# Optimization experiments

Measured on AMD Instinct MI355X. Metric: run time of the kernel, lower is better.

Reference implementation:

```python
import jax, jax.numpy as jnp
import numpy as np

TOP_K = 2


def setup_inputs() -> dict:
    key = jax.random.key(0)
    k1, k2, k3, k4 = jax.random.split(key, 4)
    B, S, H, I, E = 8, 2048, 768, 3072, 8
    x = jax.random.normal(k1, (B, S, H), dtype=jnp.float32)
    # kaiming_uniform-ish scale for weights
    router_w = jax.random.uniform(k2, (E, H), dtype=jnp.float32, minval=-1.0, maxval=1.0) * (1.0 / np.sqrt(H))
    up_w = jax.random.uniform(k3, (E, H, I), dtype=jnp.float32, minval=-1.0, maxval=1.0) * (1.0 / np.sqrt(H))
    down_w = jax.random.uniform(k4, (E, I, H), dtype=jnp.float32, minval=-1.0, maxval=1.0) * (1.0 / np.sqrt(I))
    return {"x": x, "router_w": router_w, "up_w": up_w, "down_w": down_w}


def reference(x, router_w, up_w, down_w):
    B, S, H = x.shape
    E = up_w.shape[0]
    T = B * S
    xf = x.reshape(T, H)
    # router: Linear(H -> E, bias=False) then softmax, top-k, renormalize
    logits = xf @ router_w.T                      # [T, E]
    probs = jax.nn.softmax(logits, axis=-1)
    top_w, top_i = jax.lax.top_k(probs, TOP_K)    # [T, K]
    top_w = top_w / jnp.sum(top_w, axis=-1, keepdims=True)
    # dense per-(token, expert) gate: zero for unselected experts
    gate = jnp.zeros((T, E), dtype=xf.dtype).at[jnp.arange(T)[:, None], top_i].add(top_w)
    # combine: sum_e gate[:, e] * down_e(gelu(up_e(x)))
    out = jnp.zeros_like(xf)
    for e in range(E):  # fixed small expert count; loop is structural, not over data dims
        h = jax.nn.gelu(xf @ up_w[e], approximate=False)   # exact GELU == torch F.gelu
        out = out + gate[:, e:e + 1] * (h @ down_w[e])
    return out.reshape(B, S, H)
```

## Files before the change

### kernel.cpp

```cpp
#include <hip/hip_runtime.h>

typedef short bf16x8 __attribute__((ext_vector_type(8)));
typedef float f32x4  __attribute__((ext_vector_type(4)));

#define T_TOK 16384
#define HD 768
#define ID 3072
#define NE 8
#define NT1MAX 136

__device__ __forceinline__ unsigned short f2bf(float f) {
    unsigned int u = __float_as_uint(f);
    unsigned int r = (u + 0x7FFFu + ((u >> 16) & 1u)) >> 16;
    return (unsigned short)r;
}

__device__ __forceinline__ void gload16(const void* g, void* l) {
    __builtin_amdgcn_global_load_lds(
        (const __attribute__((address_space(1))) void*)g,
        (__attribute__((address_space(3))) void*)l, 16, 0, 0);
}

__device__ __forceinline__ float gelu_f(float x) {
    float z = fabsf(x) * 0.70710678118f;
    float t = 1.0f / fmaf(0.3275911f, z, 1.0f);
    float p = t * fmaf(t, fmaf(t, fmaf(t, fmaf(t, 1.061405429f, -1.453152027f),
                                       1.421413741f), -0.284496736f), 0.254829592f);
    float e = 1.0f - p * __expf(-z * z);
    float erfv = (x >= 0.f) ? e : -e;
    return 0.5f * x * (1.0f + erfv);
}

__device__ __forceinline__ int xcd_swz(int bid, int nwg) {
    int q = nwg >> 3, rr = nwg & 7;
    int xcd = bid & 7, seq = bid >> 3;
    return (xcd < rr ? xcd * (q + 1) : rr * (q + 1) + (xcd - rr) * q) + seq;
}

__global__ __launch_bounds__(256) void k_cvt_x(const float* __restrict__ x,
                                               unsigned short* __restrict__ xb) {
    int i = blockIdx.x * 256 + threadIdx.x;
    float4 v = ((const float4*)x)[i];
    ushort4 o;
    o.x = f2bf(v.x); o.y = f2bf(v.y); o.z = f2bf(v.z); o.w = f2bf(v.w);
    ((ushort4*)xb)[i] = o;
}

__global__ __launch_bounds__(256) void k_tp(const float* __restrict__ in,
                                            unsigned short* __restrict__ out,
                                            int R, int C) {
    __shared__ float t[64][65];
    const float* ine = in + (size_t)blockIdx.z * R * C;
    unsigned short* oute = out + (size_t)blockIdx.z * R * C;
    int c0 = blockIdx.x * 64, r0 = blockIdx.y * 64;
    int lc = threadIdx.x & 63, lr4 = threadIdx.x >> 6;
#pragma unroll
    for (int i = 0; i < 16; i++) {
        int r = i * 4 + lr4;
        t[r][lc] = ine[(size_t)(r0 + r) * C + c0 + lc];
    }
    __syncthreads();
#pragma unroll
    for (int i = 0; i < 16; i++) {
        int r = i * 4 + lr4;
        oute[(size_t)(c0 + r) * R + r0 + lc] = f2bf(t[lc][r]);
    }
}

__global__ __launch_bounds__(256) void k_router(const float* __restrict__ x,
                                                const float* __restrict__ rw,
                                                int* __restrict__ topE,
                                                float* __restrict__ topW) {
    __shared__ float lrw[NE * HD];
    for (int i = threadIdx.x; i < NE * HD; i += 256) lrw[i] = rw[i];
    __syncthreads();
    int lane = threadIdx.x & 63;
    int t = blockIdx.x * 4 + (threadIdx.x >> 6);
    const float* xr = x + (size_t)t * HD;
    float acc[NE] = {0, 0, 0, 0, 0, 0, 0, 0};
    for (int h = lane; h < HD; h += 64) {
        float xv = xr[h];
#pragma unroll
        for (int e = 0; e < NE; e++) acc[e] = fmaf(xv, lrw[e * HD + h], acc[e]);
    }
#pragma unroll
    for (int e = 0; e < NE; e++) {
        float v = acc[e];
#pragma unroll
        for (int o = 32; o > 0; o >>= 1) v += __shfl_xor(v, o, 64);
        acc[e] = v;
    }
    if (lane == 0) {
        int e1 = 0; float l1 = acc[0];
#pragma unroll
        for (int e = 1; e < NE; e++) if (acc[e] > l1) { l1 = acc[e]; e1 = e; }
        int e2 = -1; float l2 = -1e30f;
#pragma unroll
        for (int e = 0; e < NE; e++) if (e != e1 && acc[e] > l2) { l2 = acc[e]; e2 = e; }
        float ex = expf(l2 - l1);
        float w1 = 1.0f / (1.0f + ex);
        topE[2 * t] = e1; topE[2 * t + 1] = e2;
        topW[2 * t] = w1; topW[2 * t + 1] = ex * w1;
    }
}

__global__ __launch_bounds__(256) void k_scatter(const int* __restrict__ topE,
                                                 const float* __restrict__ topW,
                                                 int* __restrict__ counts,
                                                 int* __restrict__ tokL,
                                                 float* __restrict__ gateL) {
    __shared__ int lc[NE], lbase[NE];
    if (threadIdx.x < NE) lc[threadIdx.x] = 0;
    __syncthreads();
    int t = blockIdx.x * 256 + threadIdx.x;
    int e1 = topE[2 * t], e2 = topE[2 * t + 1];
    int p1 = atomicAdd(&lc[e1], 1);
    int p2 = atomicAdd(&lc[e2], 1);
    __syncthreads();
    if (threadIdx.x < NE) lbase[threadIdx.x] = atomicAdd(&counts[threadIdx.x], lc[threadIdx.x]);
    __syncthreads();
    int q1 = lbase[e1] + p1, q2 = lbase[e2] + p2;
    tokL[e1 * T_TOK + q1] = t;  gateL[e1 * T_TOK + q1] = topW[2 * t];
    tokL[e2 * T_TOK + q2] = t;  gateL[e2 * T_TOK + q2] = topW[2 * t + 1];
}

__global__ void k_desc(const int* __restrict__ counts, int* __restrict__ tileE,
                       int* __restrict__ tileM0) {
    if (threadIdx.x == 0 && blockIdx.x == 0) {
        int tl = 0;
        for (int e = 0; e < NE; e++) {
            int c = counts[e];
            int nt = (c + 255) >> 8;
            for (int t = 0; t < nt; t++) { tileE[tl] = e; tileM0[tl] = t << 8; tl++; }
        }
        for (; tl < NT1MAX; tl++) { tileE[tl] = -1; tileM0[tl] = 0; }
    }
}

__global__ __launch_bounds__(512, 2) void k_gemm1(
    const unsigned short* __restrict__ xb,
    const unsigned short* __restrict__ upt,
    const int* __restrict__ tokL,
    const int* __restrict__ counts,
    const int* __restrict__ tileE,
    const int* __restrict__ tileM0,
    unsigned short* __restrict__ h,
    int seg, int ntn, int ldh) {
    __shared__ __align__(16) char lds[4][32768];
    constexpr int NK = HD / 32;
    int L = xcd_swz(blockIdx.x, gridDim.x);
    int mt = L / ntn, ntl = L - mt * ntn;
    int e = tileE[mt];
    if (e < 0) return;
    int m0 = tileM0[mt];
    int nrow = min(256, counts[e] - m0);
    const int* tok = tokL + e * T_TOK + m0;
    int n0 = (seg * ntn + ntl) * 256;

    const int tid = threadIdx.x, lane = tid & 63, wid = tid >> 6;
    const int wm = wid >> 2, wn = wid & 3;
    const int g = lane >> 4, r = lane & 15;

    int ar0 = wid * 16 + r;
    int ar1 = 128 + wid * 16 + r;
    const char* a0 = (const char*)(xb + (size_t)tok[ar0 < nrow ? ar0 : 0] * HD);
    const char* a1 = (const char*)(xb + (size_t)tok[ar1 < nrow ? ar1 : 0] * HD);
    const char* bsl = (const char*)(upt + (size_t)e * ID * HD);
    const char* b0 = bsl + (size_t)(n0 + wid * 16 + r) * (HD * 2);
    const char* b1 = bsl + (size_t)(n0 + 128 + wid * 16 + r) * (HD * 2);
    const int dst = wid * 1024;
    const int koff = g * 16;

    auto issue = [&](int step, int slot) {
        char* base = &lds[slot][0];
        int kb = step * 64 + koff;
        gload16(a0 + kb, base + dst);
        gload16(a1 + kb, base + 8192 + dst);
        gload16(b0 + kb, base + 16384 + dst);
        gload16(b1 + kb, base + 24576 + dst);
    };

    f32x4 acc[8][4];
#pragma unroll
    for (int m = 0; m < 8; m++)
#pragma unroll
        for (int n = 0; n < 4; n++) acc[m][n] = (f32x4){0.f, 0.f, 0.f, 0.f};

    issue(0, 0); issue(1, 1); issue(2, 2);
    asm volatile("s_waitcnt vmcnt(8)" ::: "memory");
    __builtin_amdgcn_s_barrier();
    asm volatile("" ::: "memory");

    const int aoff = wm * 8192 + g * 256 + r * 16;
    const int boff = 16384 + wn * 4096 + g * 256 + r * 16;

    for (int k = 0; k < NK; k++) {
        char* base = &lds[k & 3][0];
        bf16x8 a[4], b[4];
#pragma unroll
        for (int n = 0; n < 4; n++) b[n] = *(const bf16x8*)(base + boff + n * 1024);
#pragma unroll
        for (int m = 0; m < 4; m++) a[m] = *(const bf16x8*)(base + aoff + m * 1024);
        issue(min(k + 3, NK - 1), (k + 3) & 3);
        __builtin_amdgcn_s_setprio(1);
#pragma unroll
        for (int m = 0; m < 4; m++)
#pragma unroll
            for (int n = 0; n < 4; n++)
                acc[m][n] = __builtin_amdgcn_mfma_f32_16x16x32_bf16(a[m], b[n], acc[m][n], 0, 0, 0);
        __builtin_amdgcn_s_setprio(0);
#pragma unroll
        for (int m = 0; m < 4; m++) a[m] = *(const bf16x8*)(base + aoff + (4 + m) * 1024);
        __builtin_amdgcn_s_setprio(1);
#pragma unroll
        for (int m = 0; m < 4; m++)
#pragma unroll
            for (int n = 0; n < 4; n++)
                acc[4 + m][n] = __builtin_amdgcn_mfma_f32_16x16x32_bf16(a[m], b[n], acc[4 + m][n], 0, 0, 0);
        __builtin_amdgcn_s_setprio(0);
        asm volatile("s_waitcnt vmcnt(8)" ::: "memory");
        __builtin_amdgcn_s_barrier();
        asm volatile("" ::: "memory");
    }
    asm volatile("s_waitcnt vmcnt(0)" ::: "memory");

#pragma unroll
    for (int m = 0; m < 8; m++)
#pragma unroll
        for (int j = 0; j < 4; j++) {
            int rl = wm * 128 + m * 16 + g * 4 + j;
            if (rl < nrow) {
                unsigned short* hr = h + (size_t)(mt * 256 + rl) * ldh + ntl * 256 + wn * 64 + r;
#pragma unroll
                for (int n = 0; n < 4; n++) hr[n * 16] = f2bf(gelu_f(acc[m][n][j]));
            }
        }
}

__global__ __launch_bounds__(512, 2) void k_gemm2(
    const unsigned short* __restrict__ h,
    const unsigned short* __restrict__ dnt,
    const int* __restrict__ tokL,
    const float* __restrict__ gateL,
    const int* __restrict__ counts,
    const int* __restrict__ tileE,
    const int* __restrict__ tileM0,
    float* __restrict__ out,
    int seg, int ldh, int nk) {
    __shared__ __align__(16) char lds[4][32768];
    int L = xcd_swz(blockIdx.x, gridDim.x);
    int mt = L / 3, ntl = L - mt * 3;
    int e = tileE[mt];
    if (e < 0) return;
    int m0 = tileM0[mt];
    int nrow = min(256, counts[e] - m0);
    const int* tok = tokL + e * T_TOK + m0;
    const float* gat = gateL + e * T_TOK + m0;
    int n0 = ntl * 256;

    const int tid = threadIdx.x, lane = tid & 63, wid = tid >> 6;
    const int wm = wid >> 2, wn = wid & 3;
    const int g = lane >> 4, r = lane & 15;

    int ar0 = wid * 16 + r;
    int ar1 = 128 + wid * 16 + r;
    const char* a0 = (const char*)h + ((size_t)(mt * 256 + ar0) * ldh) * 2;
    const char* a1 = (const char*)h + ((size_t)(mt * 256 + ar1) * ldh) * 2;
    const char* bsl = (const char*)(dnt + (size_t)e * ID * HD) + (size_t)seg * ldh * 2;
    const char* b0 = bsl + (size_t)(n0 + wid * 16 + r) * (ID * 2);
    const char* b1 = bsl + (size_t)(n0 + 128 + wid * 16 + r) * (ID * 2);
    const int dst = wid * 1024;
    const int koff = g * 16;

    auto issue = [&](int step, int slot) {
        char* base = &lds[slot][0];
        int kb = step * 64 + koff;
        gload16(a0 + kb, base + dst);
        gload16(a1 + kb, base + 8192 + dst);
        gload16(b0 + kb, base + 16384 + dst);
        gload16(b1 + kb, base + 24576 + dst);
    };

    f32x4 acc[8][4];
#pragma unroll
    for (int m = 0; m < 8; m++)
#pragma unroll
        for (int n = 0; n < 4; n++) acc[m][n] = (f32x4){0.f, 0.f, 0.f, 0.f};

    issue(0, 0); issue(1, 1); issue(2, 2);
    asm volatile("s_waitcnt vmcnt(8)" ::: "memory");
    __builtin_amdgcn_s_barrier();
    asm volatile("" ::: "memory");

    const int aoff = wm * 8192 + g * 256 + r * 16;
    const int boff = 16384 + wn * 4096 + g * 256 + r * 16;

    for (int k = 0; k < nk; k++) {
        char* base = &lds[k & 3][0];
        bf16x8 a[4], b[4];
#pragma unroll
        for (int n = 0; n < 4; n++) b[n] = *(const bf16x8*)(base + boff + n * 1024);
#pragma unroll
        for (int m = 0; m < 4; m++) a[m] = *(const bf16x8*)(base + aoff + m * 1024);
        issue(min(k + 3, nk - 1), (k + 3) & 3);
        __builtin_amdgcn_s_setprio(1);
#pragma unroll
        for (int m = 0; m < 4; m++)
#pragma unroll
            for (int n = 0; n < 4; n++)
                acc[m][n] = __builtin_amdgcn_mfma_f32_16x16x32_bf16(a[m], b[n], acc[m][n], 0, 0, 0);
        __builtin_amdgcn_s_setprio(0);
#pragma unroll
        for (int m = 0; m < 4; m++) a[m] = *(const bf16x8*)(base + aoff + (4 + m) * 1024);
        __builtin_amdgcn_s_setprio(1);
#pragma unroll
        for (int m = 0; m < 4; m++)
#pragma unroll
            for (int n = 0; n < 4; n++)
                acc[4 + m][n] = __builtin_amdgcn_mfma_f32_16x16x32_bf16(a[m], b[n], acc[4 + m][n], 0, 0, 0);
        __builtin_amdgcn_s_setprio(0);
        asm volatile("s_waitcnt vmcnt(8)" ::: "memory");
        __builtin_amdgcn_s_barrier();
        asm volatile("" ::: "memory");
    }
    asm volatile("s_waitcnt vmcnt(0)" ::: "memory");

#pragma unroll
    for (int m = 0; m < 8; m++)
#pragma unroll
        for (int j = 0; j < 4; j++) {
            int rl = wm * 128 + m * 16 + g * 4 + j;
            if (rl < nrow) {
                int t = tok[rl];
                float gv = gat[rl];
                float* orow = out + (size_t)t * HD + n0 + wn * 64 + r;
#pragma unroll
                for (int n = 0; n < 4; n++)
                    atomicAdd(orow + n * 16, gv * acc[m][n][j]);
            }
        }
}

__global__ __launch_bounds__(512, 2) void k_moe(
    const unsigned short* __restrict__ xb,
    const unsigned short* __restrict__ upt,
    const unsigned short* __restrict__ dnt,
    const int* __restrict__ counts,
    const int* __restrict__ tokL,
    const float* __restrict__ gateL,
    float* __restrict__ out) {
    __shared__ __align__(16) char lds[155648];
    char* xs = lds;
    char* hs = lds + 98304;
    char* ring = lds + 106496;

    const int e = blockIdx.x & 7;
    const int slot = blockIdx.x >> 3;
    const int cnt = counts[e];
    if (slot * 64 >= cnt) return;
    const int nrow = min(64, cnt - slot * 64);
    const int* tok = tokL + e * T_TOK + slot * 64;
    const float* gat = gateL + e * T_TOK + slot * 64;

    const int tid = threadIdx.x;
    const int lane = tid & 63;
    const int wid = tid >> 6;
    const int mi = wid >> 2, ni = wid & 3;

    const char* upe = (const char*)(upt + (size_t)e * ID * HD);
    const char* dne = (const char*)(dnt + (size_t)e * HD * ID);

    {
        int off = tid * 16;
#pragma unroll
        for (int s = 0; s < 12; s++) {
            int o = off + s * 8192;
            int m = o / 1536;
            int cb = o - m * 1536;
            int tk = (m < nrow) ? tok[m] : tok[0];
            const char* src = (const char*)xb + (size_t)tk * 1536 + (size_t)(cb ^ ((m & 7) << 4));
            gload16(src, xs + s * 8192 + wid * 1024);
        }
    }
    asm volatile("s_waitcnt vmcnt(0)" ::: "memory");
    __builtin_amdgcn_s_barrier();
    asm volatile("" ::: "memory");

    auto issue = [&](int s) {
        char* dst = ring + (s % 6) * 8192 + wid * 1024;
        int ci = s / 24;
        int ph = s - ci * 24;
        int row = tid >> 3;
        int cb = (tid & 7) << 4;
        int scb = cb ^ ((row & 7) << 4);
        const char* src;
        if (ci >= 48) src = upe;
        else if (ph < 12) src = upe + (size_t)(ci * 64 + row) * 1536 + ph * 128 + scb;
        else              src = dne + (size_t)((ph - 12) * 64 + row) * 6144 + ci * 128 + scb;
        gload16(src, dst);
    };

    f32x4 acc[2][12];
#pragma unroll
    for (int a = 0; a < 2; a++)
#pragma unroll
        for (int b = 0; b < 12; b++) acc[a][b] = (f32x4){0.f, 0.f, 0.f, 0.f};

    issue(0); issue(1); issue(2); issue(3);

    f32x4 acch[2];
    bf16x8 ha[2][2];

    for (int ci = 0; ci < 48; ci++) {
#pragma unroll
        for (int ks = 0; ks < 12; ks++) {
            issue(ci * 24 + ks + 4);
            asm volatile("s_waitcnt vmcnt(4)" ::: "memory");
            __builtin_amdgcn_s_barrier();
            asm volatile("" ::: "memory");
            char* buf = ring + (ks % 6) * 8192;
            if (ks == 0) { acch[0] = (f32x4){0.f,0.f,0.f,0.f}; acch[1] = (f32x4){0.f,0.f,0.f,0.f}; }
#pragma unroll
            for (int kr = 0; kr < 2; kr++) {
                int bn = ni * 16 + (lane & 15);
                int bo = ((kr * 32 + (lane >> 4) * 8) * 2) ^ ((bn & 7) << 4);
                bf16x8 bfrag = *(const bf16x8*)(buf + bn * 128 + bo);
#pragma unroll
                for (int mr = 0; mr < 2; mr++) {
                    int ar = mi * 32 + mr * 16 + (lane & 15);
                    int ao = ((ks * 64 + kr * 32 + (lane >> 4) * 8) * 2) ^ ((ar & 7) << 4);
                    bf16x8 afrag = *(const bf16x8*)(xs + ar * 1536 + ao);
                    acch[mr] = __builtin_amdgcn_mfma_f32_16x16x32_bf16(afrag, bfrag, acch[mr], 0, 0, 0);
                }
            }
            if (ks == 11) {
#pragma unroll
                for (int mr = 0; mr < 2; mr++) {
                    int col = ni * 16 + (lane & 15);
#pragma unroll
                    for (int r = 0; r < 4; r++) {
                        int m = mi * 32 + mr * 16 + (lane >> 4) * 4 + r;
                        float v = acch[mr][r];
                        *(unsigned short*)(hs + m * 128 + ((col * 2) ^ ((m & 7) << 4))) = f2bf(gelu_f(v));
                    }
                }
                asm volatile("s_waitcnt lgkmcnt(0)" ::: "memory");
            }
        }
#pragma unroll
        for (int j = 0; j < 12; j++) {
            issue(ci * 24 + 12 + j + 4);
            asm volatile("s_waitcnt vmcnt(4)" ::: "memory");
            __builtin_amdgcn_s_barrier();
            asm volatile("" ::: "memory");
            char* buf = ring + ((12 + j) % 6) * 8192;
            if (j == 0) {
#pragma unroll
                for (int mr = 0; mr < 2; mr++)
#pragma unroll
                    for (int kr = 0; kr < 2; kr++) {
                        int ar = mi * 32 + mr * 16 + (lane & 15);
                        int ao = ((kr * 32 + (lane >> 4) * 8) * 2) ^ ((ar & 7) << 4);
                        ha[mr][kr] = *(const bf16x8*)(hs + ar * 128 + ao);
                    }
            }
#pragma unroll
            for (int kr = 0; kr < 2; kr++) {
                int bn = ni * 16 + (lane & 15);
                int bo = ((kr * 32 + (lane >> 4) * 8) * 2) ^ ((bn & 7) << 4);
                bf16x8 bfrag = *(const bf16x8*)(buf + bn * 128 + bo);
#pragma unroll
                for (int mr = 0; mr < 2; mr++)
                    acc[mr][j] = __builtin_amdgcn_mfma_f32_16x16x32_bf16(ha[mr][kr], bfrag, acc[mr][j], 0, 0, 0);
            }
        }
    }

    int   t4[2][4];
    float g4[2][4];
#pragma unroll
    for (int mr = 0; mr < 2; mr++)
#pragma unroll
        for (int r = 0; r < 4; r++) {
            int m = mi * 32 + mr * 16 + (lane >> 4) * 4 + r;
            bool valid = m < nrow;
            t4[mr][r] = valid ? tok[m] : -1;
            g4[mr][r] = valid ? gat[m] : 0.f;
        }
#pragma unroll
    for (int mr = 0; mr < 2; mr++)
#pragma unroll
        for (int j = 0; j < 12; j++) {
            int colg = j * 64 + ni * 16 + (lane & 15);
#pragma unroll
            for (int r = 0; r < 4; r++) {
                if (t4[mr][r] >= 0)
                    atomicAdd(out + (size_t)t4[mr][r] * HD + colg, g4[mr][r] * acc[mr][j][r]);
            }
        }
}

extern "C" void kernel_launch(void* const* d_in, const int* in_sizes, int n_in,
                              void* d_out, int out_size, void* d_ws, size_t ws_size,
                              hipStream_t stream) {
    const float* x  = (const float*)d_in[0];
    const float* rw = (const float*)d_in[1];
    const float* uw = (const float*)d_in[2];
    const float* dw = (const float*)d_in[3];
    float* out = (float*)d_out;

    size_t off = 0;
    char* base = (char*)d_ws;
    auto alloc = [&](size_t bytes) -> char* {
        char* p = base + off;
        off += (bytes + 1023) & ~(size_t)1023;
        return p;
    };
    unsigned short* xb   = (unsigned short*)alloc((size_t)T_TOK * HD * 2);
    unsigned short* upt  = (unsigned short*)alloc((size_t)NE * ID * HD * 2);
    unsigned short* dnt  = (unsigned short*)alloc((size_t)NE * HD * ID * 2);
    int*   topE   = (int*)alloc((size_t)T_TOK * 2 * 4);
    float* topW   = (float*)alloc((size_t)T_TOK * 2 * 4);
    int*   counts = (int*)alloc(256);
    int*   tileE  = (int*)alloc(NT1MAX * 4);
    int*   tileM0 = (int*)alloc(NT1MAX * 4);
    int*   tokL   = (int*)alloc((size_t)NE * T_TOK * 4);
    float* gateL  = (float*)alloc((size_t)NE * T_TOK * 4);
    size_t fixed = off;

    const int cand[6] = {1, 2, 3, 4, 6, 12};
    int S = 0;
    size_t hrows = (size_t)NT1MAX * 256;
    for (int i = 0; i < 6; i++) {
        size_t hb = hrows * (ID / cand[i]) * 2;
        if (fixed + hb <= ws_size) { S = cand[i]; break; }
    }
    unsigned short* h = (unsigned short*)(base + fixed);

    hipMemsetAsync(d_out, 0, (size_t)T_TOK * HD * 4, stream);
    hipMemsetAsync(counts, 0, 256, stream);

    k_cvt_x<<<(T_TOK * HD) / (256 * 4), 256, 0, stream>>>(x, xb);
    k_tp<<<dim3(ID / 64, HD / 64, NE), 256, 0, stream>>>(uw, upt, HD, ID);
    k_tp<<<dim3(HD / 64, ID / 64, NE), 256, 0, stream>>>(dw, dnt, ID, HD);
    k_router<<<T_TOK / 4, 256, 0, stream>>>(x, rw, topE, topW);
    k_scatter<<<T_TOK / 256, 256, 0, stream>>>(topE, topW, counts, tokL, gateL);

    if (S > 0) {
        int ntn = 12 / S;
        int ldh = ID / S;
        int nk2 = ldh / 32;
        k_desc<<<1, 64, 0, stream>>>(counts, tileE, tileM0);
        for (int sg = 0; sg < S; sg++) {
            k_gemm1<<<NT1MAX * ntn, 512, 0, stream>>>(xb, upt, tokL, counts, tileE, tileM0,
                                                      h, sg, ntn, ldh);
            k_gemm2<<<NT1MAX * 3, 512, 0, stream>>>(h, dnt, tokL, gateL, counts, tileE, tileM0,
                                                    out, sg, ldh, nk2);
        }
    } else {
        k_moe<<<2048, 512, 0, stream>>>(xb, upt, dnt, counts, tokL, gateL, out);
    }
}
```

Before: 775.6 us.

## Shrink grouped GEMM tiles to 128x128 with single-buffered 64-wide K steps

Both expert GEMM kernels switch from 256x256 tiles with 512 threads and a 4-stage async LDS pipeline to 128x128 tiles with 256 threads, a single 32KB LDS buffer and K steps of 64. This reduces padding waste on partial expert tiles and raises occupancy to three blocks per CU. In exchange it drops the prefetch pipelining, since each step waits for all loads before computing, and it lowers per-tile data reuse, which increases global traffic.

```diff
diff --git a/kernel.cpp b/kernel.cpp
--- a/kernel.cpp
+++ b/kernel.cpp
@@ -7,7 +7,7 @@
 #define HD 768
 #define ID 3072
 #define NE 8
-#define NT1MAX 136
+#define NTM 264
 
 __device__ __forceinline__ unsigned short f2bf(float f) {
     unsigned int u = __float_as_uint(f);
@@ -130,14 +130,14 @@
         int tl = 0;
         for (int e = 0; e < NE; e++) {
             int c = counts[e];
-            int nt = (c + 255) >> 8;
-            for (int t = 0; t < nt; t++) { tileE[tl] = e; tileM0[tl] = t << 8; tl++; }
-        }
-        for (; tl < NT1MAX; tl++) { tileE[tl] = -1; tileM0[tl] = 0; }
-    }
-}
-
-__global__ __launch_bounds__(512, 2) void k_gemm1(
+            int nt = (c + 127) >> 7;
+            for (int t = 0; t < nt; t++) { tileE[tl] = e; tileM0[tl] = t << 7; tl++; }
+        }
+        for (; tl < NTM; tl++) { tileE[tl] = -1; tileM0[tl] = 0; }
+    }
+}
+
+__global__ __launch_bounds__(256, 3) void k_gemm1(
     const unsigned short* __restrict__ xb,
     const unsigned short* __restrict__ upt,
     const int* __restrict__ tokL,
@@ -145,99 +145,85 @@
     const int* __restrict__ tileE,
     const int* __restrict__ tileM0,
     unsigned short* __restrict__ h,
-    int seg, int ntn, int ldh) {
-    __shared__ __align__(16) char lds[4][32768];
-    constexpr int NK = HD / 32;
+    int segI, int ntn, int ldh) {
+    __shared__ __align__(16) char lds[32768];
+    constexpr int NK = HD / 64;
     int L = xcd_swz(blockIdx.x, gridDim.x);
     int mt = L / ntn, ntl = L - mt * ntn;
     int e = tileE[mt];
     if (e < 0) return;
     int m0 = tileM0[mt];
-    int nrow = min(256, counts[e] - m0);
+    int nrow = min(128, counts[e] - m0);
     const int* tok = tokL + e * T_TOK + m0;
-    int n0 = (seg * ntn + ntl) * 256;
 
     const int tid = threadIdx.x, lane = tid & 63, wid = tid >> 6;
-    const int wm = wid >> 2, wn = wid & 3;
+    const int wm = wid >> 1, wn = wid & 1;
     const int g = lane >> 4, r = lane & 15;
 
-    int ar0 = wid * 16 + r;
-    int ar1 = 128 + wid * 16 + r;
-    const char* a0 = (const char*)(xb + (size_t)tok[ar0 < nrow ? ar0 : 0] * HD);
-    const char* a1 = (const char*)(xb + (size_t)tok[ar1 < nrow ? ar1 : 0] * HD);
     const char* bsl = (const char*)(upt + (size_t)e * ID * HD);
-    const char* b0 = bsl + (size_t)(n0 + wid * 16 + r) * (HD * 2);
-    const char* b1 = bsl + (size_t)(n0 + 128 + wid * 16 + r) * (HD * 2);
-    const int dst = wid * 1024;
-    const int koff = g * 16;
-
-    auto issue = [&](int step, int slot) {
-        char* base = &lds[slot][0];
-        int kb = step * 64 + koff;
-        gload16(a0 + kb, base + dst);
-        gload16(a1 + kb, base + 8192 + dst);
-        gload16(b0 + kb, base + 16384 + dst);
-        gload16(b1 + kb, base + 24576 + dst);
-    };
-
-    f32x4 acc[8][4];
-#pragma unroll
-    for (int m = 0; m < 8; m++)
+    const char* asrc[4];
+    const char* bsrc[4];
+#pragma unroll
+    for (int j = 0; j < 4; j++) {
+        int c = wid * 4 + j;
+        int row = (c >> 1) * 16 + r;
+        int kb0 = (c & 1) * 64 + g * 16;
+        asrc[j] = (const char*)xb + (size_t)tok[row < nrow ? row : 0] * (HD * 2) + kb0;
+        bsrc[j] = bsl + (size_t)(segI + ntl * 128 + row) * (HD * 2) + kb0;
+    }
+    const int dst = wid * 4096;
+
+    f32x4 acc[4][4];
+#pragma unroll
+    for (int m = 0; m < 4; m++)
 #pragma unroll
         for (int n = 0; n < 4; n++) acc[m][n] = (f32x4){0.f, 0.f, 0.f, 0.f};
 
-    issue(0, 0); issue(1, 1); issue(2, 2);
-    asm volatile("s_waitcnt vmcnt(8)" ::: "memory");
-    __builtin_amdgcn_s_barrier();
-    asm volatile("" ::: "memory");
-
-    const int aoff = wm * 8192 + g * 256 + r * 16;
-    const int boff = 16384 + wn * 4096 + g * 256 + r * 16;
+    const int foff = g * 256 + r * 16;
 
     for (int k = 0; k < NK; k++) {
-        char* base = &lds[k & 3][0];
-        bf16x8 a[4], b[4];
-#pragma unroll
-        for (int n = 0; n < 4; n++) b[n] = *(const bf16x8*)(base + boff + n * 1024);
-#pragma unroll
-        for (int m = 0; m < 4; m++) a[m] = *(const bf16x8*)(base + aoff + m * 1024);
-        issue(min(k + 3, NK - 1), (k + 3) & 3);
-        __builtin_amdgcn_s_setprio(1);
-#pragma unroll
-        for (int m = 0; m < 4; m++)
-#pragma unroll
-            for (int n = 0; n < 4; n++)
-                acc[m][n] = __builtin_amdgcn_mfma_f32_16x16x32_bf16(a[m], b[n], acc[m][n], 0, 0, 0);
-        __builtin_amdgcn_s_setprio(0);
-#pragma unroll
-        for (int m = 0; m < 4; m++) a[m] = *(const bf16x8*)(base + aoff + (4 + m) * 1024);
-        __builtin_amdgcn_s_setprio(1);
-#pragma unroll
-        for (int m = 0; m < 4; m++)
-#pragma unroll
-            for (int n = 0; n < 4; n++)
-                acc[4 + m][n] = __builtin_amdgcn_mfma_f32_16x16x32_bf16(a[m], b[n], acc[4 + m][n], 0, 0, 0);
-        __builtin_amdgcn_s_setprio(0);
-        asm volatile("s_waitcnt vmcnt(8)" ::: "memory");
+#pragma unroll
+        for (int j = 0; j < 4; j++) gload16(asrc[j], lds + dst + j * 1024);
+#pragma unroll
+        for (int j = 0; j < 4; j++) gload16(bsrc[j], lds + 16384 + dst + j * 1024);
+        asm volatile("s_waitcnt vmcnt(0)" ::: "memory");
         __builtin_amdgcn_s_barrier();
         asm volatile("" ::: "memory");
-    }
-    asm volatile("s_waitcnt vmcnt(0)" ::: "memory");
-
-#pragma unroll
-    for (int m = 0; m < 8; m++)
+#pragma unroll
+        for (int kh = 0; kh < 2; kh++) {
+            bf16x8 a[4], b[4];
+#pragma unroll
+            for (int n = 0; n < 4; n++)
+                b[n] = *(const bf16x8*)(lds + 16384 + ((wn * 4 + n) * 2 + kh) * 1024 + foff);
+#pragma unroll
+            for (int m = 0; m < 4; m++)
+                a[m] = *(const bf16x8*)(lds + ((wm * 4 + m) * 2 + kh) * 1024 + foff);
+#pragma unroll
+            for (int m = 0; m < 4; m++)
+#pragma unroll
+                for (int n = 0; n < 4; n++)
+                    acc[m][n] = __builtin_amdgcn_mfma_f32_16x16x32_bf16(a[m], b[n], acc[m][n], 0, 0, 0);
+        }
+        __builtin_amdgcn_s_barrier();
+        asm volatile("" ::: "memory");
+#pragma unroll
+        for (int j = 0; j < 4; j++) { asrc[j] += 128; bsrc[j] += 128; }
+    }
+
+#pragma unroll
+    for (int m = 0; m < 4; m++)
 #pragma unroll
         for (int j = 0; j < 4; j++) {
-            int rl = wm * 128 + m * 16 + g * 4 + j;
+            int rl = wm * 64 + m * 16 + g * 4 + j;
             if (rl < nrow) {
-                unsigned short* hr = h + (size_t)(mt * 256 + rl) * ldh + ntl * 256 + wn * 64 + r;
+                unsigned short* hr = h + (size_t)(mt * 128 + rl) * ldh + ntl * 128 + wn * 64 + r;
 #pragma unroll
                 for (int n = 0; n < 4; n++) hr[n * 16] = f2bf(gelu_f(acc[m][n][j]));
             }
         }
 }
 
-__global__ __launch_bounds__(512, 2) void k_gemm2(
+__global__ __launch_bounds__(256, 3) void k_gemm2(
     const unsigned short* __restrict__ h,
     const unsigned short* __restrict__ dnt,
     const int* __restrict__ tokL,
@@ -246,90 +232,77 @@
     const int* __restrict__ tileE,
     const int* __restrict__ tileM0,
     float* __restrict__ out,
-    int seg, int ldh, int nk) {
-    __shared__ __align__(16) char lds[4][32768];
+    int segI, int ldh, int nk) {
+    __shared__ __align__(16) char lds[32768];
     int L = xcd_swz(blockIdx.x, gridDim.x);
-    int mt = L / 3, ntl = L - mt * 3;
+    int mt = L / 6, ntl = L - mt * 6;
     int e = tileE[mt];
     if (e < 0) return;
     int m0 = tileM0[mt];
-    int nrow = min(256, counts[e] - m0);
+    int nrow = min(128, counts[e] - m0);
     const int* tok = tokL + e * T_TOK + m0;
     const float* gat = gateL + e * T_TOK + m0;
-    int n0 = ntl * 256;
+    int n0 = ntl * 128;
 
     const int tid = threadIdx.x, lane = tid & 63, wid = tid >> 6;
-    const int wm = wid >> 2, wn = wid & 3;
+    const int wm = wid >> 1, wn = wid & 1;
     const int g = lane >> 4, r = lane & 15;
 
-    int ar0 = wid * 16 + r;
-    int ar1 = 128 + wid * 16 + r;
-    const char* a0 = (const char*)h + ((size_t)(mt * 256 + ar0) * ldh) * 2;
-    const char* a1 = (const char*)h + ((size_t)(mt * 256 + ar1) * ldh) * 2;
-    const char* bsl = (const char*)(dnt + (size_t)e * ID * HD) + (size_t)seg * ldh * 2;
-    const char* b0 = bsl + (size_t)(n0 + wid * 16 + r) * (ID * 2);
-    const char* b1 = bsl + (size_t)(n0 + 128 + wid * 16 + r) * (ID * 2);
-    const int dst = wid * 1024;
-    const int koff = g * 16;
-
-    auto issue = [&](int step, int slot) {
-        char* base = &lds[slot][0];
-        int kb = step * 64 + koff;
-        gload16(a0 + kb, base + dst);
-        gload16(a1 + kb, base + 8192 + dst);
-        gload16(b0 + kb, base + 16384 + dst);
-        gload16(b1 + kb, base + 24576 + dst);
-    };
-
-    f32x4 acc[8][4];
-#pragma unroll
-    for (int m = 0; m < 8; m++)
+    const char* bsl = (const char*)(dnt + (size_t)e * ID * HD) + (size_t)segI * 2;
+    const char* asrc[4];
+    const char* bsrc[4];
+#pragma unroll
+    for (int j = 0; j < 4; j++) {
+        int c = wid * 4 + j;
+        int row = (c >> 1) * 16 + r;
+        int kb0 = (c & 1) * 64 + g * 16;
+        asrc[j] = (const char*)h + ((size_t)(mt * 128 + row) * ldh) * 2 + kb0;
+        bsrc[j] = bsl + (size_t)(n0 + row) * (ID * 2) + kb0;
+    }
+    const int dst = wid * 4096;
+
+    f32x4 acc[4][4];
+#pragma unroll
+    for (int m = 0; m < 4; m++)
 #pragma unroll
         for (int n = 0; n < 4; n++) acc[m][n] = (f32x4){0.f, 0.f, 0.f, 0.f};
 
-    issue(0, 0); issue(1, 1); issue(2, 2);
-    asm volatile("s_waitcnt vmcnt(8)" ::: "memory");
-    __builtin_amdgcn_s_barrier();
-    asm volatile("" ::: "memory");
-
-    const int aoff = wm * 8192 + g * 256 + r * 16;
-    const int boff = 16384 + wn * 4096 + g * 256 + r * 16;
+    const int foff = g * 256 + r * 16;
 
     for (int k = 0; k < nk; k++) {
-        char* base = &lds[k & 3][0];
-        bf16x8 a[4], b[4];
-#pragma unroll
-        for (int n = 0; n < 4; n++) b[n] = *(const bf16x8*)(base + boff + n * 1024);
-#pragma unroll
-        for (int m = 0; m < 4; m++) a[m] = *(const bf16x8*)(base + aoff + m * 1024);
-        issue(min(k + 3, nk - 1), (k + 3) & 3);
-        __builtin_amdgcn_s_setprio(1);
-#pragma unroll
-        for (int m = 0; m < 4; m++)
-#pragma unroll
-            for (int n = 0; n < 4; n++)
-                acc[m][n] = __builtin_amdgcn_mfma_f32_16x16x32_bf16(a[m], b[n], acc[m][n], 0, 0, 0);
-        __builtin_amdgcn_s_setprio(0);
-#pragma unroll
-        for (int m = 0; m < 4; m++) a[m] = *(const bf16x8*)(base + aoff + (4 + m) * 1024);
-        __builtin_amdgcn_s_setprio(1);
-#pragma unroll
-        for (int m = 0; m < 4; m++)
-#pragma unroll
-            for (int n = 0; n < 4; n++)
-                acc[4 + m][n] = __builtin_amdgcn_mfma_f32_16x16x32_bf16(a[m], b[n], acc[4 + m][n], 0, 0, 0);
-        __builtin_amdgcn_s_setprio(0);
-        asm volatile("s_waitcnt vmcnt(8)" ::: "memory");
+#pragma unroll
+        for (int j = 0; j < 4; j++) gload16(asrc[j], lds + dst + j * 1024);
+#pragma unroll
+        for (int j = 0; j < 4; j++) gload16(bsrc[j], lds + 16384 + dst + j * 1024);
+        asm volatile("s_waitcnt vmcnt(0)" ::: "memory");
         __builtin_amdgcn_s_barrier();
         asm volatile("" ::: "memory");
-    }
-    asm volatile("s_waitcnt vmcnt(0)" ::: "memory");
-
-#pragma unroll
-    for (int m = 0; m < 8; m++)
+#pragma unroll
+        for (int kh = 0; kh < 2; kh++) {
+            bf16x8 a[4], b[4];
+#pragma unroll
+            for (int n = 0; n < 4; n++)
+                b[n] = *(const bf16x8*)(lds + 16384 + ((wn * 4 + n) * 2 + kh) * 1024 + foff);
+#pragma unroll
+            for (int m = 0; m < 4; m++)
+                a[m] = *(const bf16x8*)(lds + ((wm * 4 + m) * 2 + kh) * 1024 + foff);
+#pragma unroll
+            for (int m = 0; m < 4; m++)
+#pragma unroll
+                for (int n = 0; n < 4; n++)
+                    acc[m][n] = __builtin_amdgcn_mfma_f32_16x16x32_bf16(a[m], b[n], acc[m][n], 0, 0, 0);
+        }
+        __builtin_amdgcn_s_barrier();
+        asm volatile("" ::: "memory");
+#pragma unroll
+        for (int j = 0; j < 4; j++) { asrc[j] += 128; bsrc[j] += 128; }
+    }
+
+#pragma unroll
+    for (int m = 0; m < 4; m++)
 #pragma unroll
         for (int j = 0; j < 4; j++) {
-            int rl = wm * 128 + m * 16 + g * 4 + j;
+            int rl = wm * 64 + m * 16 + g * 4 + j;
             if (rl < nrow) {
                 int t = tok[rl];
                 float gv = gat[rl];
@@ -522,15 +495,15 @@
     int*   topE   = (int*)alloc((size_t)T_TOK * 2 * 4);
     float* topW   = (float*)alloc((size_t)T_TOK * 2 * 4);
     int*   counts = (int*)alloc(256);
-    int*   tileE  = (int*)alloc(NT1MAX * 4);
-    int*   tileM0 = (int*)alloc(NT1MAX * 4);
+    int*   tileE  = (int*)alloc(NTM * 4);
+    int*   tileM0 = (int*)alloc(NTM * 4);
     int*   tokL   = (int*)alloc((size_t)NE * T_TOK * 4);
     float* gateL  = (float*)alloc((size_t)NE * T_TOK * 4);
     size_t fixed = off;
 
     const int cand[6] = {1, 2, 3, 4, 6, 12};
     int S = 0;
-    size_t hrows = (size_t)NT1MAX * 256;
+    size_t hrows = (size_t)NTM * 128;
     for (int i = 0; i < 6; i++) {
         size_t hb = hrows * (ID / cand[i]) * 2;
         if (fixed + hb <= ws_size) { S = cand[i]; break; }
@@ -547,15 +520,15 @@
     k_scatter<<<T_TOK / 256, 256, 0, stream>>>(topE, topW, counts, tokL, gateL);
 
     if (S > 0) {
-        int ntn = 12 / S;
         int ldh = ID / S;
-        int nk2 = ldh / 32;
+        int ntn = ldh / 128;
+        int nk2 = ldh / 64;
         k_desc<<<1, 64, 0, stream>>>(counts, tileE, tileM0);
         for (int sg = 0; sg < S; sg++) {
-            k_gemm1<<<NT1MAX * ntn, 512, 0, stream>>>(xb, upt, tokL, counts, tileE, tileM0,
-                                                      h, sg, ntn, ldh);
-            k_gemm2<<<NT1MAX * 3, 512, 0, stream>>>(h, dnt, tokL, gateL, counts, tileE, tileM0,
-                                                    out, sg, ldh, nk2);
+            k_gemm1<<<NTM * ntn, 256, 0, stream>>>(xb, upt, tokL, counts, tileE, tileM0,
+                                                   h, sg * ldh, ntn, ldh);
+            k_gemm2<<<NTM * 6, 256, 0, stream>>>(h, dnt, tokL, gateL, counts, tileE, tileM0,
+                                                 out, sg * ldh, ldh, nk2);
         }
     } else {
         k_moe<<<2048, 512, 0, stream>>>(xb, upt, dnt, counts, tokL, gateL, out);
```

Measured after the change: 809.5 us. +4.4%, slower.

## Restructure grouped GEMM mainloops into double-buffered 64-wide K tiles with staged loads

Applied to the files above, without the earlier changes.

Both grouped GEMM kernels move from a 4-slot ring of 32-wide K steps to a 2-parity double buffer of 64-wide K tiles, 128 KB of LDS in total. Each tile is split into four MFMA phases, with barriers and lgkmcnt waits between them and the next tile's A/B global-to-LDS loads issued in pieces across those phases. The aim is to halve the number of K-loop iterations and interleave memory traffic with MFMA work, a schedule in the style of HipKittens 8-wave kernels. The cost is many more barriers per iteration. Doubling LDS per block to 128 KB may also cut occupancy below the 2 blocks per CU requested by the launch bounds.

```diff
diff --git a/kernel.cpp b/kernel.cpp
--- a/kernel.cpp
+++ b/kernel.cpp
@@ -146,8 +146,8 @@
     const int* __restrict__ tileM0,
     unsigned short* __restrict__ h,
     int seg, int ntn, int ldh) {
-    __shared__ __align__(16) char lds[4][32768];
-    constexpr int NK = HD / 32;
+    __shared__ __align__(16) char lds[131072];
+    constexpr int NKT = HD / 64;
     int L = xcd_swz(blockIdx.x, gridDim.x);
     int mt = L / ntn, ntl = L - mt * ntn;
     int e = tileE[mt];
@@ -160,25 +160,33 @@
     const int tid = threadIdx.x, lane = tid & 63, wid = tid >> 6;
     const int wm = wid >> 2, wn = wid & 3;
     const int g = lane >> 4, r = lane & 15;
-
-    int ar0 = wid * 16 + r;
-    int ar1 = 128 + wid * 16 + r;
-    const char* a0 = (const char*)(xb + (size_t)tok[ar0 < nrow ? ar0 : 0] * HD);
-    const char* a1 = (const char*)(xb + (size_t)tok[ar1 < nrow ? ar1 : 0] * HD);
+    const int kr = wid & 1;
+
     const char* bsl = (const char*)(upt + (size_t)e * ID * HD);
-    const char* b0 = bsl + (size_t)(n0 + wid * 16 + r) * (HD * 2);
-    const char* b1 = bsl + (size_t)(n0 + 128 + wid * 16 + r) * (HD * 2);
-    const int dst = wid * 1024;
-    const int koff = g * 16;
-
-    auto issue = [&](int step, int slot) {
-        char* base = &lds[slot][0];
-        int kb = step * 64 + koff;
-        gload16(a0 + kb, base + dst);
-        gload16(a1 + kb, base + 8192 + dst);
-        gload16(b0 + kb, base + 16384 + dst);
-        gload16(b1 + kb, base + 24576 + dst);
+    const char* aB[2][2];
+    const char* bB[2][2];
+#pragma unroll
+    for (int hh = 0; hh < 2; hh++)
+#pragma unroll
+        for (int j = 0; j < 2; j++) {
+            int row = (hh * 8 + j * 4 + (wid >> 1)) * 16 + r;
+            aB[hh][j] = (const char*)xb + (size_t)tok[row < nrow ? row : 0] * (HD * 2) + kr * 64 + g * 16;
+            bB[hh][j] = bsl + (size_t)(n0 + row) * (HD * 2) + kr * 64 + g * 16;
+        }
+
+    auto stgA = [&](int T_, int hh_) {
+        int p_ = (T_ & 1) * 65536;
+        gload16(aB[hh_][0] + T_ * 128, lds + p_ + (hh_ * 16 + wid) * 1024);
+        gload16(aB[hh_][1] + T_ * 128, lds + p_ + (hh_ * 16 + 8 + wid) * 1024);
     };
+    auto stgB = [&](int T_, int hh_) {
+        int p_ = (T_ & 1) * 65536 + 32768;
+        gload16(bB[hh_][0] + T_ * 128, lds + p_ + (hh_ * 16 + wid) * 1024);
+        gload16(bB[hh_][1] + T_ * 128, lds + p_ + (hh_ * 16 + 8 + wid) * 1024);
+    };
+    const int foff = g * 256 + r * 16;
+    auto AO = [&](int mf, int krr, int par) { return par * 65536 + ((wm * 8 + mf) * 2 + krr) * 1024 + foff; };
+    auto BO = [&](int nf, int krr, int par) { return par * 65536 + 32768 + ((wn * 4 + nf) * 2 + krr) * 1024 + foff; };
 
     f32x4 acc[8][4];
 #pragma unroll
@@ -186,22 +194,23 @@
 #pragma unroll
         for (int n = 0; n < 4; n++) acc[m][n] = (f32x4){0.f, 0.f, 0.f, 0.f};
 
-    issue(0, 0); issue(1, 1); issue(2, 2);
-    asm volatile("s_waitcnt vmcnt(8)" ::: "memory");
+    stgB(0, 0); stgB(0, 1); stgA(0, 0); stgA(0, 1); stgB(1, 0);
+    asm volatile("s_waitcnt vmcnt(2)" ::: "memory");
     __builtin_amdgcn_s_barrier();
     asm volatile("" ::: "memory");
 
-    const int aoff = wm * 8192 + g * 256 + r * 16;
-    const int boff = 16384 + wn * 4096 + g * 256 + r * 16;
-
-    for (int k = 0; k < NK; k++) {
-        char* base = &lds[k & 3][0];
-        bf16x8 a[4], b[4];
-#pragma unroll
-        for (int n = 0; n < 4; n++) b[n] = *(const bf16x8*)(base + boff + n * 1024);
-#pragma unroll
-        for (int m = 0; m < 4; m++) a[m] = *(const bf16x8*)(base + aoff + m * 1024);
-        issue(min(k + 3, NK - 1), (k + 3) & 3);
+    bf16x8 a[4], b[4];
+    for (int T = 0; T < NKT; ++T) {
+        int par = T & 1;
+#pragma unroll
+        for (int i = 0; i < 4; i++) a[i] = *(const bf16x8*)(lds + AO(i, 0, par));
+#pragma unroll
+        for (int i = 0; i < 4; i++) b[i] = *(const bf16x8*)(lds + BO(i, 0, par));
+        if (T + 1 < NKT) { stgB(T + 1, 1); stgA(T + 1, 0); }
+        asm volatile("" ::: "memory");
+        __builtin_amdgcn_s_barrier();
+        asm volatile("s_waitcnt lgkmcnt(0)" ::: "memory");
+        __builtin_amdgcn_sched_barrier(0);
         __builtin_amdgcn_s_setprio(1);
 #pragma unroll
         for (int m = 0; m < 4; m++)
@@ -209,8 +218,15 @@
             for (int n = 0; n < 4; n++)
                 acc[m][n] = __builtin_amdgcn_mfma_f32_16x16x32_bf16(a[m], b[n], acc[m][n], 0, 0, 0);
         __builtin_amdgcn_s_setprio(0);
-#pragma unroll
-        for (int m = 0; m < 4; m++) a[m] = *(const bf16x8*)(base + aoff + (4 + m) * 1024);
+        asm volatile("" ::: "memory");
+        __builtin_amdgcn_s_barrier();
+#pragma unroll
+        for (int i = 0; i < 4; i++) a[i] = *(const bf16x8*)(lds + AO(4 + i, 0, par));
+        if (T + 1 < NKT) stgA(T + 1, 1);
+        asm volatile("" ::: "memory");
+        __builtin_amdgcn_s_barrier();
+        asm volatile("s_waitcnt lgkmcnt(0)" ::: "memory");
+        __builtin_amdgcn_sched_barrier(0);
         __builtin_amdgcn_s_setprio(1);
 #pragma unroll
         for (int m = 0; m < 4; m++)
@@ -218,21 +234,53 @@
             for (int n = 0; n < 4; n++)
                 acc[4 + m][n] = __builtin_amdgcn_mfma_f32_16x16x32_bf16(a[m], b[n], acc[4 + m][n], 0, 0, 0);
         __builtin_amdgcn_s_setprio(0);
-        asm volatile("s_waitcnt vmcnt(8)" ::: "memory");
-        __builtin_amdgcn_s_barrier();
-        asm volatile("" ::: "memory");
+        asm volatile("" ::: "memory");
+        __builtin_amdgcn_s_barrier();
+#pragma unroll
+        for (int i = 0; i < 4; i++) a[i] = *(const bf16x8*)(lds + AO(i, 1, par));
+#pragma unroll
+        for (int i = 0; i < 4; i++) b[i] = *(const bf16x8*)(lds + BO(i, 1, par));
+        asm volatile("" ::: "memory");
+        __builtin_amdgcn_s_barrier();
+        asm volatile("s_waitcnt lgkmcnt(0)" ::: "memory");
+        __builtin_amdgcn_sched_barrier(0);
+        __builtin_amdgcn_s_setprio(1);
+#pragma unroll
+        for (int m = 0; m < 4; m++)
+#pragma unroll
+            for (int n = 0; n < 4; n++)
+                acc[m][n] = __builtin_amdgcn_mfma_f32_16x16x32_bf16(a[m], b[n], acc[m][n], 0, 0, 0);
+        __builtin_amdgcn_s_setprio(0);
+        asm volatile("" ::: "memory");
+        __builtin_amdgcn_s_barrier();
+#pragma unroll
+        for (int i = 0; i < 4; i++) a[i] = *(const bf16x8*)(lds + AO(4 + i, 1, par));
+        { int Ts = (T + 2 < NKT) ? T + 2 : NKT - 1; stgB(Ts, 0); }
+        asm volatile("s_waitcnt vmcnt(2)" ::: "memory");
+        __builtin_amdgcn_s_barrier();
+        asm volatile("s_waitcnt lgkmcnt(0)" ::: "memory");
+        __builtin_amdgcn_sched_barrier(0);
+        __builtin_amdgcn_s_setprio(1);
+#pragma unroll
+        for (int m = 0; m < 4; m++)
+#pragma unroll
+            for (int n = 0; n < 4; n++)
+                acc[4 + m][n] = __builtin_amdgcn_mfma_f32_16x16x32_bf16(a[m], b[n], acc[4 + m][n], 0, 0, 0);
+        __builtin_amdgcn_s_setprio(0);
+        asm volatile("" ::: "memory");
+        __builtin_amdgcn_s_barrier();
     }
     asm volatile("s_waitcnt vmcnt(0)" ::: "memory");
 
 #pragma unroll
     for (int m = 0; m < 8; m++)
 #pragma unroll
-        for (int j = 0; j < 4; j++) {
-            int rl = wm * 128 + m * 16 + g * 4 + j;
+        for (int jj = 0; jj < 4; jj++) {
+            int rl = wm * 128 + m * 16 + g * 4 + jj;
             if (rl < nrow) {
                 unsigned short* hr = h + (size_t)(mt * 256 + rl) * ldh + ntl * 256 + wn * 64 + r;
 #pragma unroll
-                for (int n = 0; n < 4; n++) hr[n * 16] = f2bf(gelu_f(acc[m][n][j]));
+                for (int n = 0; n < 4; n++) hr[n * 16] = f2bf(gelu_f(acc[m][n][jj]));
             }
         }
 }
@@ -246,8 +294,8 @@
     const int* __restrict__ tileE,
     const int* __restrict__ tileM0,
     float* __restrict__ out,
-    int seg, int ldh, int nk) {
-    __shared__ __align__(16) char lds[4][32768];
+    int seg, int ldh, int nkt) {
+    __shared__ __align__(16) char lds[131072];
     int L = xcd_swz(blockIdx.x, gridDim.x);
     int mt = L / 3, ntl = L - mt * 3;
     int e = tileE[mt];
@@ -261,25 +309,33 @@
     const int tid = threadIdx.x, lane = tid & 63, wid = tid >> 6;
     const int wm = wid >> 2, wn = wid & 3;
     const int g = lane >> 4, r = lane & 15;
-
-    int ar0 = wid * 16 + r;
-    int ar1 = 128 + wid * 16 + r;
-    const char* a0 = (const char*)h + ((size_t)(mt * 256 + ar0) * ldh) * 2;
-    const char* a1 = (const char*)h + ((size_t)(mt * 256 + ar1) * ldh) * 2;
+    const int kr = wid & 1;
+
     const char* bsl = (const char*)(dnt + (size_t)e * ID * HD) + (size_t)seg * ldh * 2;
-    const char* b0 = bsl + (size_t)(n0 + wid * 16 + r) * (ID * 2);
-    const char* b1 = bsl + (size_t)(n0 + 128 + wid * 16 + r) * (ID * 2);
-    const int dst = wid * 1024;
-    const int koff = g * 16;
-
-    auto issue = [&](int step, int slot) {
-        char* base = &lds[slot][0];
-        int kb = step * 64 + koff;
-        gload16(a0 + kb, base + dst);
-        gload16(a1 + kb, base + 8192 + dst);
-        gload16(b0 + kb, base + 16384 + dst);
-        gload16(b1 + kb, base + 24576 + dst);
+    const char* aB[2][2];
+    const char* bB[2][2];
+#pragma unroll
+    for (int hh = 0; hh < 2; hh++)
+#pragma unroll
+        for (int j = 0; j < 2; j++) {
+            int row = (hh * 8 + j * 4 + (wid >> 1)) * 16 + r;
+            aB[hh][j] = (const char*)h + (size_t)(mt * 256 + row) * ldh * 2 + kr * 64 + g * 16;
+            bB[hh][j] = bsl + (size_t)(n0 + row) * (ID * 2) + kr * 64 + g * 16;
+        }
+
+    auto stgA = [&](int T_, int hh_) {
+        int p_ = (T_ & 1) * 65536;
+        gload16(aB[hh_][0] + T_ * 128, lds + p_ + (hh_ * 16 + wid) * 1024);
+        gload16(aB[hh_][1] + T_ * 128, lds + p_ + (hh_ * 16 + 8 + wid) * 1024);
     };
+    auto stgB = [&](int T_, int hh_) {
+        int p_ = (T_ & 1) * 65536 + 32768;
+        gload16(bB[hh_][0] + T_ * 128, lds + p_ + (hh_ * 16 + wid) * 1024);
+        gload16(bB[hh_][1] + T_ * 128, lds + p_ + (hh_ * 16 + 8 + wid) * 1024);
+    };
+    const int foff = g * 256 + r * 16;
+    auto AO = [&](int mf, int krr, int par) { return par * 65536 + ((wm * 8 + mf) * 2 + krr) * 1024 + foff; };
+    auto BO = [&](int nf, int krr, int par) { return par * 65536 + 32768 + ((wn * 4 + nf) * 2 + krr) * 1024 + foff; };
 
     f32x4 acc[8][4];
 #pragma unroll
@@ -287,22 +343,23 @@
 #pragma unroll
         for (int n = 0; n < 4; n++) acc[m][n] = (f32x4){0.f, 0.f, 0.f, 0.f};
 
-    issue(0, 0); issue(1, 1); issue(2, 2);
-    asm volatile("s_waitcnt vmcnt(8)" ::: "memory");
+    stgB(0, 0); stgB(0, 1); stgA(0, 0); stgA(0, 1); stgB(1, 0);
+    asm volatile("s_waitcnt vmcnt(2)" ::: "memory");
     __builtin_amdgcn_s_barrier();
     asm volatile("" ::: "memory");
 
-    const int aoff = wm * 8192 + g * 256 + r * 16;
-    const int boff = 16384 + wn * 4096 + g * 256 + r * 16;
-
-    for (int k = 0; k < nk; k++) {
-        char* base = &lds[k & 3][0];
-        bf16x8 a[4], b[4];
-#pragma unroll
-        for (int n = 0; n < 4; n++) b[n] = *(const bf16x8*)(base + boff + n * 1024);
-#pragma unroll
-        for (int m = 0; m < 4; m++) a[m] = *(const bf16x8*)(base + aoff + m * 1024);
-        issue(min(k + 3, nk - 1), (k + 3) & 3);
+    bf16x8 a[4], b[4];
+    for (int T = 0; T < nkt; ++T) {
+        int par = T & 1;
+#pragma unroll
+        for (int i = 0; i < 4; i++) a[i] = *(const bf16x8*)(lds + AO(i, 0, par));
+#pragma unroll
+        for (int i = 0; i < 4; i++) b[i] = *(const bf16x8*)(lds + BO(i, 0, par));
+        if (T + 1 < nkt) { stgB(T + 1, 1); stgA(T + 1, 0); }
+        asm volatile("" ::: "memory");
+        __builtin_amdgcn_s_barrier();
+        asm volatile("s_waitcnt lgkmcnt(0)" ::: "memory");
+        __builtin_amdgcn_sched_barrier(0);
         __builtin_amdgcn_s_setprio(1);
 #pragma unroll
         for (int m = 0; m < 4; m++)
@@ -310,8 +367,15 @@
             for (int n = 0; n < 4; n++)
                 acc[m][n] = __builtin_amdgcn_mfma_f32_16x16x32_bf16(a[m], b[n], acc[m][n], 0, 0, 0);
         __builtin_amdgcn_s_setprio(0);
-#pragma unroll
-        for (int m = 0; m < 4; m++) a[m] = *(const bf16x8*)(base + aoff + (4 + m) * 1024);
+        asm volatile("" ::: "memory");
+        __builtin_amdgcn_s_barrier();
+#pragma unroll
+        for (int i = 0; i < 4; i++) a[i] = *(const bf16x8*)(lds + AO(4 + i, 0, par));
+        if (T + 1 < nkt) stgA(T + 1, 1);
+        asm volatile("" ::: "memory");
+        __builtin_amdgcn_s_barrier();
+        asm volatile("s_waitcnt lgkmcnt(0)" ::: "memory");
+        __builtin_amdgcn_sched_barrier(0);
         __builtin_amdgcn_s_setprio(1);
 #pragma unroll
         for (int m = 0; m < 4; m++)
@@ -319,24 +383,56 @@
             for (int n = 0; n < 4; n++)
                 acc[4 + m][n] = __builtin_amdgcn_mfma_f32_16x16x32_bf16(a[m], b[n], acc[4 + m][n], 0, 0, 0);
         __builtin_amdgcn_s_setprio(0);
-        asm volatile("s_waitcnt vmcnt(8)" ::: "memory");
-        __builtin_amdgcn_s_barrier();
-        asm volatile("" ::: "memory");
+        asm volatile("" ::: "memory");
+        __builtin_amdgcn_s_barrier();
+#pragma unroll
+        for (int i = 0; i < 4; i++) a[i] = *(const bf16x8*)(lds + AO(i, 1, par));
+#pragma unroll
+        for (int i = 0; i < 4; i++) b[i] = *(const bf16x8*)(lds + BO(i, 1, par));
+        asm volatile("" ::: "memory");
+        __builtin_amdgcn_s_barrier();
+        asm volatile("s_waitcnt lgkmcnt(0)" ::: "memory");
+        __builtin_amdgcn_sched_barrier(0);
+        __builtin_amdgcn_s_setprio(1);
+#pragma unroll
+        for (int m = 0; m < 4; m++)
+#pragma unroll
+            for (int n = 0; n < 4; n++)
+                acc[m][n] = __builtin_amdgcn_mfma_f32_16x16x32_bf16(a[m], b[n], acc[m][n], 0, 0, 0);
+        __builtin_amdgcn_s_setprio(0);
+        asm volatile("" ::: "memory");
+        __builtin_amdgcn_s_barrier();
+#pragma unroll
+        for (int i = 0; i < 4; i++) a[i] = *(const bf16x8*)(lds + AO(4 + i, 1, par));
+        { int Ts = (T + 2 < nkt) ? T + 2 : nkt - 1; stgB(Ts, 0); }
+        asm volatile("s_waitcnt vmcnt(2)" ::: "memory");
+        __builtin_amdgcn_s_barrier();
+        asm volatile("s_waitcnt lgkmcnt(0)" ::: "memory");
+        __builtin_amdgcn_sched_barrier(0);
+        __builtin_amdgcn_s_setprio(1);
+#pragma unroll
+        for (int m = 0; m < 4; m++)
+#pragma unroll
+            for (int n = 0; n < 4; n++)
+                acc[4 + m][n] = __builtin_amdgcn_mfma_f32_16x16x32_bf16(a[m], b[n], acc[4 + m][n], 0, 0, 0);
+        __builtin_amdgcn_s_setprio(0);
+        asm volatile("" ::: "memory");
+        __builtin_amdgcn_s_barrier();
     }
     asm volatile("s_waitcnt vmcnt(0)" ::: "memory");
 
 #pragma unroll
     for (int m = 0; m < 8; m++)
 #pragma unroll
-        for (int j = 0; j < 4; j++) {
-            int rl = wm * 128 + m * 16 + g * 4 + j;
+        for (int jj = 0; jj < 4; jj++) {
+            int rl = wm * 128 + m * 16 + g * 4 + jj;
             if (rl < nrow) {
                 int t = tok[rl];
                 float gv = gat[rl];
                 float* orow = out + (size_t)t * HD + n0 + wn * 64 + r;
 #pragma unroll
                 for (int n = 0; n < 4; n++)
-                    atomicAdd(orow + n * 16, gv * acc[m][n][j]);
+                    atomicAdd(orow + n * 16, gv * acc[m][n][jj]);
             }
         }
 }
@@ -421,14 +517,14 @@
             char* buf = ring + (ks % 6) * 8192;
             if (ks == 0) { acch[0] = (f32x4){0.f,0.f,0.f,0.f}; acch[1] = (f32x4){0.f,0.f,0.f,0.f}; }
 #pragma unroll
-            for (int kr = 0; kr < 2; kr++) {
+            for (int kkr = 0; kkr < 2; kkr++) {
                 int bn = ni * 16 + (lane & 15);
-                int bo = ((kr * 32 + (lane >> 4) * 8) * 2) ^ ((bn & 7) << 4);
+                int bo = ((kkr * 32 + (lane >> 4) * 8) * 2) ^ ((bn & 7) << 4);
                 bf16x8 bfrag = *(const bf16x8*)(buf + bn * 128 + bo);
 #pragma unroll
                 for (int mr = 0; mr < 2; mr++) {
                     int ar = mi * 32 + mr * 16 + (lane & 15);
-                    int ao = ((ks * 64 + kr * 32 + (lane >> 4) * 8) * 2) ^ ((ar & 7) << 4);
+                    int ao = ((ks * 64 + kkr * 32 + (lane >> 4) * 8) * 2) ^ ((ar & 7) << 4);
                     bf16x8 afrag = *(const bf16x8*)(xs + ar * 1536 + ao);
                     acch[mr] = __builtin_amdgcn_mfma_f32_16x16x32_bf16(afrag, bfrag, acch[mr], 0, 0, 0);
                 }
@@ -438,9 +534,9 @@
                 for (int mr = 0; mr < 2; mr++) {
                     int col = ni * 16 + (lane & 15);
 #pragma unroll
-                    for (int r = 0; r < 4; r++) {
-                        int m = mi * 32 + mr * 16 + (lane >> 4) * 4 + r;
-                        float v = acch[mr][r];
+                    for (int rr = 0; rr < 4; rr++) {
+                        int m = mi * 32 + mr * 16 + (lane >> 4) * 4 + rr;
+                        float v = acch[mr][rr];
                         *(unsigned short*)(hs + m * 128 + ((col * 2) ^ ((m & 7) << 4))) = f2bf(gelu_f(v));
                     }
                 }
@@ -458,20 +554,20 @@
 #pragma unroll
                 for (int mr = 0; mr < 2; mr++)
 #pragma unroll
-                    for (int kr = 0; kr < 2; kr++) {
+                    for (int kkr = 0; kkr < 2; kkr++) {
                         int ar = mi * 32 + mr * 16 + (lane & 15);
-                        int ao = ((kr * 32 + (lane >> 4) * 8) * 2) ^ ((ar & 7) << 4);
-                        ha[mr][kr] = *(const bf16x8*)(hs + ar * 128 + ao);
+                        int ao = ((kkr * 32 + (lane >> 4) * 8) * 2) ^ ((ar & 7) << 4);
+                        ha[mr][kkr] = *(const bf16x8*)(hs + ar * 128 + ao);
                     }
             }
 #pragma unroll
-            for (int kr = 0; kr < 2; kr++) {
+            for (int kkr = 0; kkr < 2; kkr++) {
                 int bn = ni * 16 + (lane & 15);
-                int bo = ((kr * 32 + (lane >> 4) * 8) * 2) ^ ((bn & 7) << 4);
+                int bo = ((kkr * 32 + (lane >> 4) * 8) * 2) ^ ((bn & 7) << 4);
                 bf16x8 bfrag = *(const bf16x8*)(buf + bn * 128 + bo);
 #pragma unroll
                 for (int mr = 0; mr < 2; mr++)
-                    acc[mr][j] = __builtin_amdgcn_mfma_f32_16x16x32_bf16(ha[mr][kr], bfrag, acc[mr][j], 0, 0, 0);
+                    acc[mr][j] = __builtin_amdgcn_mfma_f32_16x16x32_bf16(ha[mr][kkr], bfrag, acc[mr][j], 0, 0, 0);
             }
         }
     }
@@ -481,11 +577,11 @@
 #pragma unroll
     for (int mr = 0; mr < 2; mr++)
 #pragma unroll
-        for (int r = 0; r < 4; r++) {
-            int m = mi * 32 + mr * 16 + (lane >> 4) * 4 + r;
+        for (int rr = 0; rr < 4; rr++) {
+            int m = mi * 32 + mr * 16 + (lane >> 4) * 4 + rr;
             bool valid = m < nrow;
-            t4[mr][r] = valid ? tok[m] : -1;
-            g4[mr][r] = valid ? gat[m] : 0.f;
+            t4[mr][rr] = valid ? tok[m] : -1;
+            g4[mr][rr] = valid ? gat[m] : 0.f;
         }
 #pragma unroll
     for (int mr = 0; mr < 2; mr++)
@@ -493,9 +589,9 @@
         for (int j = 0; j < 12; j++) {
             int colg = j * 64 + ni * 16 + (lane & 15);
 #pragma unroll
-            for (int r = 0; r < 4; r++) {
-                if (t4[mr][r] >= 0)
-                    atomicAdd(out + (size_t)t4[mr][r] * HD + colg, g4[mr][r] * acc[mr][j][r]);
+            for (int rr = 0; rr < 4; rr++) {
+                if (t4[mr][rr] >= 0)
+                    atomicAdd(out + (size_t)t4[mr][rr] * HD + colg, g4[mr][rr] * acc[mr][j][rr]);
             }
         }
 }
@@ -547,15 +643,15 @@
     k_scatter<<<T_TOK / 256, 256, 0, stream>>>(topE, topW, counts, tokL, gateL);
 
     if (S > 0) {
-        int ntn = 12 / S;
         int ldh = ID / S;
-        int nk2 = ldh / 32;
+        int ntn = ldh / 256;
+        int nkt = ldh / 64;
         k_desc<<<1, 64, 0, stream>>>(counts, tileE, tileM0);
         for (int sg = 0; sg < S; sg++) {
             k_gemm1<<<NT1MAX * ntn, 512, 0, stream>>>(xb, upt, tokL, counts, tileE, tileM0,
                                                       h, sg, ntn, ldh);
             k_gemm2<<<NT1MAX * 3, 512, 0, stream>>>(h, dnt, tokL, gateL, counts, tileE, tileM0,
-                                                    out, sg, ldh, nk2);
+                                                    out, sg, ldh, nkt);
         }
     } else {
         k_moe<<<2048, 512, 0, stream>>>(xb, upt, dnt, counts, tokL, gateL, out);
```

Measured after the change: 790.9 us. About the same (+2.0%).
